# Kernel tuning notes

Measured on AMD Instinct MI355X. Metric: run time of the kernel, lower is better.

## Reference

```python
import jax, jax.numpy as jnp
import numpy as np

S, B, D, H = 2048, 2, 2048, 16
HD = D // H  # 128
EPS = 1e-5


def _layernorm(x, w, b):
    mu = jnp.mean(x, axis=-1, keepdims=True)
    var = jnp.mean((x - mu) ** 2, axis=-1, keepdims=True)
    return (x - mu) * jax.lax.rsqrt(var + EPS) * w + b


def _apply_rotary(x, freqs_cis):
    # x: [B, S, H, HD]; freqs_cis: [S, HD//2, 2]
    xr = x.astype(jnp.float32).reshape(x.shape[0], x.shape[1], x.shape[2], HD // 2, 2)
    f = freqs_cis.reshape(1, xr.shape[1], 1, xr.shape[3], 2)
    out = jnp.stack(
        [xr[..., 0] * f[..., 0] - xr[..., 1] * f[..., 1],
         xr[..., 1] * f[..., 0] + xr[..., 0] * f[..., 1]],
        axis=-1,
    )
    return out.reshape(x.shape).astype(x.dtype)


def setup_inputs() -> dict:
    key = jax.random.key(0)
    ks = jax.random.split(key, 6)
    scale = 0.02
    return {
        "x": jax.random.normal(ks[0], (S, B, D), dtype=jnp.float32),
        "freqs_cis": jax.random.normal(ks[1], (S, HD // 2, 2), dtype=jnp.float32),
        "wqkv_w": jax.random.normal(ks[2], (3 * D, D), dtype=jnp.float32) * scale,
        "wqkv_b": jnp.zeros((3 * D,), dtype=jnp.float32),
        "wo_w": jax.random.normal(ks[3], (D, D), dtype=jnp.float32) * scale,
        "wo_b": jnp.zeros((D,), dtype=jnp.float32),
        "qn_w": jnp.ones((HD,), dtype=jnp.float32),
        "qn_b": jnp.zeros((HD,), dtype=jnp.float32),
        "kn_w": jnp.ones((HD,), dtype=jnp.float32),
        "kn_b": jnp.zeros((HD,), dtype=jnp.float32),
    }


def reference(x, freqs_cis, wqkv_w, wqkv_b, wo_w, wo_b, qn_w, qn_b, kn_w, kn_b):
    # x: [S, B, D] -> [B, S, D]
    xb = jnp.transpose(x, (1, 0, 2))
    qkv = jnp.einsum("bsd,ed->bse", xb, wqkv_w) + wqkv_b  # [B, S, 3D]
    xq, xk, xv = jnp.split(qkv, 3, axis=-1)
    xq = xq.reshape(B, S, H, HD)
    xk = xk.reshape(B, S, H, HD)
    xv = xv.reshape(B, S, H, HD)
    # QK-norm over head_dim
    xq = _layernorm(xq, qn_w, qn_b)
    xk = _layernorm(xk, kn_w, kn_b)
    # RoPE
    xq = _apply_rotary(xq, freqs_cis)
    xk = _apply_rotary(xk, freqs_cis)
    # [B, H, S, HD]
    q = jnp.transpose(xq, (0, 2, 1, 3))
    k = jnp.transpose(xk, (0, 2, 1, 3))
    v = jnp.transpose(xv, (0, 2, 1, 3))
    scores = jnp.einsum("bhqd,bhkd->bhqk", q, k) / jnp.sqrt(jnp.float32(HD))
    causal = jnp.tril(jnp.ones((S, S), dtype=bool))
    scores = jnp.where(causal, scores, jnp.finfo(scores.dtype).min)
    attn = jax.nn.softmax(scores, axis=-1)
    out = jnp.einsum("bhqk,bhkd->bhqd", attn, v)  # [B, H, S, HD]
    out = jnp.transpose(out, (0, 2, 1, 3)).reshape(B, S, D)
    out = jnp.einsum("bsd,ed->bse", out, wo_w) + wo_b
    return jnp.transpose(out, (1, 0, 2))  # [S, B, D]
```

## Files before the change

kernel.cpp:

```cpp
#include <hip/hip_runtime.h>
#include <hip/hip_bf16.h>

#define S 2048
#define B 2
#define D 2048
#define H 16
#define HD 128
#define N3 6144
#define KD 2048

typedef __hip_bfloat16 bf16;
typedef float f32x4 __attribute__((ext_vector_type(4)));
typedef short short8 __attribute__((ext_vector_type(8)));
typedef short sv4 __attribute__((ext_vector_type(4)));

__device__ __forceinline__ void gload16(const void* g, void* l) {
    __builtin_amdgcn_global_load_lds((const __attribute__((address_space(1))) void*)g,
                                     (__attribute__((address_space(3))) void*)l, 16, 0, 0);
}
__device__ __forceinline__ void bar() {
    asm volatile("" ::: "memory");
    __builtin_amdgcn_s_barrier();
    asm volatile("" ::: "memory");
}

__global__ __launch_bounds__(256) void cvt_x_kernel(const float* __restrict__ x, bf16* __restrict__ xb) {
    int i = blockIdx.x * 256 + threadIdx.x;
    int d  = i & (D - 1);
    int sb = i >> 11;
    int b  = sb & (B - 1);
    int s  = sb >> 1;
    xb[((size_t)(b * S + s) << 11) + d] = __float2bfloat16(x[i]);
}

__global__ __launch_bounds__(256) void cvt_w_kernel(const float* __restrict__ in, bf16* __restrict__ o, int n) {
    for (int i = blockIdx.x * blockDim.x + threadIdx.x; i < n; i += gridDim.x * blockDim.x)
        o[i] = __float2bfloat16(in[i]);
}

template <int MODE>
__global__ __launch_bounds__(256, 2) void gemm128(
    const bf16* __restrict__ A, const bf16* __restrict__ W, const float* __restrict__ bias,
    bf16* __restrict__ oq, bf16* __restrict__ ok, bf16* __restrict__ ovT,
    float* __restrict__ oOut)
{
    constexpr int NT = KD / 64;

    __shared__ __align__(16) bf16 SA[2][128 * 64];
    __shared__ __align__(16) bf16 SB[2][128 * 64];

    const int tid = threadIdx.x;
    const int w = tid >> 6, l = tid & 63;
    const int wm = w >> 1, wn = w & 1;
    const int l15 = l & 15, l4 = l >> 4;

    const int nwg = gridDim.x * gridDim.y;
    const int id  = blockIdx.y * gridDim.x + blockIdx.x;
    const int nid = (id & 7) * (nwg >> 3) + (id >> 3);
    const int tileN = (nid % gridDim.x) * 128;
    const int tileM = (nid / gridDim.x) * 128;

    const int lrow8 = l >> 3;
    const int lsb   = ((l & 7) * 16) ^ (lrow8 << 4);
    const int rxor  = (l15 & 7) << 3;

    const char* AgT = (const char*)A + (size_t)tileM * (KD * 2);
    const char* WgT = (const char*)W + (size_t)tileN * (KD * 2);

    auto stage_tile = [&](int buf, int kt) {
#pragma unroll
        for (int j = 0; j < 4; ++j) {
            const int chunk = w * 4 + j;
            gload16(AgT + (size_t)(chunk * 8 + lrow8) * (KD * 2) + kt * 128 + lsb,
                    (char*)&SA[buf][0] + chunk * 1024);
        }
#pragma unroll
        for (int j = 0; j < 4; ++j) {
            const int chunk = w * 4 + j;
            gload16(WgT + (size_t)(chunk * 8 + lrow8) * (KD * 2) + kt * 128 + lsb,
                    (char*)&SB[buf][0] + chunk * 1024);
        }
    };

    f32x4 acc[4][4] = {};

#define TILE_BODY(BUF, KTN)                                                                \
    {                                                                                      \
        stage_tile(BUF ^ 1, KTN);                                                          \
        _Pragma("unroll") for (int kk = 0; kk < 2; ++kk) {                                 \
            short8 bfrag[4], afr[4];                                                       \
            _Pragma("unroll") for (int ni = 0; ni < 4; ++ni)                               \
                bfrag[ni] = *(const short8*)&SB[BUF][(wn * 64 + ni * 16 + l15) * 64 +      \
                                                     ((kk * 32 + l4 * 8) ^ rxor)];         \
            _Pragma("unroll") for (int q = 0; q < 4; ++q)                                  \
                afr[q] = *(const short8*)&SA[BUF][(wm * 64 + q * 16 + l15) * 64 +          \
                                                  ((kk * 32 + l4 * 8) ^ rxor)];            \
            __builtin_amdgcn_s_setprio(1);                                                 \
            _Pragma("unroll") for (int q = 0; q < 4; ++q)                                  \
                _Pragma("unroll") for (int ni = 0; ni < 4; ++ni)                           \
                    acc[q][ni] = __builtin_amdgcn_mfma_f32_16x16x32_bf16(                  \
                        afr[q], bfrag[ni], acc[q][ni], 0, 0, 0);                           \
            __builtin_amdgcn_s_setprio(0);                                                 \
        }                                                                                  \
        asm volatile("s_waitcnt vmcnt(0)" ::: "memory");                                   \
        bar();                                                                             \
    }

    stage_tile(0, 0);
    asm volatile("s_waitcnt vmcnt(0)" ::: "memory");
    bar();

#pragma unroll 1
    for (int t = 0; t < NT; t += 2) {
        const int tn1 = (t + 1 < NT) ? t + 1 : NT - 1;
        const int tn2 = (t + 2 < NT) ? t + 2 : NT - 1;
        TILE_BODY(0, tn1)
        TILE_BODY(1, tn2)
    }
#undef TILE_BODY

#pragma unroll
    for (int mi = 0; mi < 4; ++mi) {
#pragma unroll
        for (int ni = 0; ni < 4; ++ni) {
            const int ncol = tileN + wn * 64 + ni * 16 + l15;
            const float bv = bias[ncol];
            const int m0 = tileM + wm * 64 + mi * 16 + l4 * 4;
            if (MODE == 0) {
                const int b_ = m0 >> 11, s0 = m0 & (S - 1);
                const int which = ncol >> 11;
                const int hh = (ncol >> 7) & (H - 1);
                const int hd = ncol & (HD - 1);
                const int bh = b_ * H + hh;
                if (which == 2) {
                    sv4 pk;
#pragma unroll
                    for (int r = 0; r < 4; ++r) {
                        __hip_bfloat16 t = __float2bfloat16(acc[mi][ni][r] + bv);
                        pk[r] = reinterpret_cast<short&>(t);
                    }
                    *(sv4*)&ovT[((size_t)bh * HD + hd) * S + s0] = pk;
                } else {
                    bf16* dst = which ? ok : oq;
#pragma unroll
                    for (int r = 0; r < 4; ++r)
                        dst[((size_t)bh * S + s0 + r) * HD + hd] =
                            __float2bfloat16(acc[mi][ni][r] + bv);
                }
            } else {
#pragma unroll
                for (int r = 0; r < 4; ++r) {
                    const int m = m0 + r;
                    const int b_ = m >> 11, s_ = m & (S - 1);
                    oOut[((size_t)s_ * B + b_) * D + ncol] = acc[mi][ni][r] + bv;
                }
            }
        }
    }
}

__global__ __launch_bounds__(256) void ln_rope_kernel(
    bf16* __restrict__ q, bf16* __restrict__ k,
    const float* __restrict__ fc,
    const float* __restrict__ qw, const float* __restrict__ qb,
    const float* __restrict__ kw, const float* __restrict__ kb)
{
    const int tid = threadIdx.x;
    const int w = tid >> 6, l = tid & 63;
    const int row = blockIdx.x * 4 + w;
    const int s_ = row & (S - 1);
    const size_t base = (size_t)row * HD;
    const float f0 = fc[s_ * HD + 2 * l];
    const float f1 = fc[s_ * HD + 2 * l + 1];

#pragma unroll
    for (int which = 0; which < 2; ++which) {
        bf16* p = which == 0 ? q : k;
        const float* gw = which == 0 ? qw : kw;
        const float* gb = which == 0 ? qb : kb;
        const float osc = which == 0 ? 0.08838834764831845f : 1.0f;
        float x0 = __bfloat162float(p[base + 2 * l]);
        float x1 = __bfloat162float(p[base + 2 * l + 1]);
        float sm = x0 + x1;
#pragma unroll
        for (int msk = 1; msk < 64; msk <<= 1) sm += __shfl_xor(sm, msk);
        const float mu = sm * (1.0f / HD);
        const float d0 = x0 - mu, d1 = x1 - mu;
        float vs = d0 * d0 + d1 * d1;
#pragma unroll
        for (int msk = 1; msk < 64; msk <<= 1) vs += __shfl_xor(vs, msk);
        const float rstd = rsqrtf(vs * (1.0f / HD) + 1e-5f);
        const float n0 = d0 * rstd * gw[2 * l] + gb[2 * l];
        const float n1 = d1 * rstd * gw[2 * l + 1] + gb[2 * l + 1];
        p[base + 2 * l]     = __float2bfloat16((n0 * f0 - n1 * f1) * osc);
        p[base + 2 * l + 1] = __float2bfloat16((n1 * f0 + n0 * f1) * osc);
    }
}

__global__ __launch_bounds__(256, 2) void attn_kernel(
    const bf16* __restrict__ q, const bf16* __restrict__ k, const bf16* __restrict__ vT,
    bf16* __restrict__ out)
{
    __shared__ __align__(16) bf16 KT[2][64 * 128];
    __shared__ __align__(16) bf16 VS[2][128 * 64];
    __shared__ __align__(16) bf16 Pb[4][16 * 72];

    const int tid = threadIdx.x, w = tid >> 6, l = tid & 63;
    const int l15 = l & 15, l4 = l >> 4;

    const int id  = blockIdx.y * gridDim.x + blockIdx.x;
    const int nid = (id & 7) * 128 + (id >> 3);
    const int bh  = nid >> 5;
    const int qt  = 31 - (nid & 31);

    const int b_ = bh >> 4, hh = bh & (H - 1);
    const int qbase = qt * 64;
    const int qr0 = qbase + w * 16;
    const size_t hQ = (size_t)bh * S * HD;
    const size_t hV = (size_t)bh * HD * S;

    const char* kbase = (const char*)(k + hQ);
    const char* vbase = (const char*)(vT + hV);
    int ksrc[4], vsrc[4], kdst[4], vdst[4];
#pragma unroll
    for (int j = 0; j < 4; ++j) {
        const int ik = w * 4 + j;
        const int rt = ik * 4 + (l >> 4);
        ksrc[j] = rt * 256 + (((l & 15) * 16) ^ ((rt & 15) << 4));
        kdst[j] = ik * 1024;
        const int rd = ik * 8 + (l >> 3);
        vsrc[j] = rd * (S * 2) + (((l & 7) * 16) ^ ((rd & 7) << 4));
        vdst[j] = ik * 1024;
    }

    short8 aq[4];
#pragma unroll
    for (int c = 0; c < 4; ++c)
        aq[c] = *(const short8*)&q[hQ + (size_t)(qr0 + l15) * HD + c * 32 + l4 * 8];

    f32x4 o[8] = {};
    float psum[4] = {0.0f, 0.0f, 0.0f, 0.0f};

#pragma unroll
    for (int j = 0; j < 4; ++j)
        gload16(kbase + ksrc[j], (char*)KT[0] + kdst[j]);

    const int kx = l15 << 3;
    const int vx = (l15 & 7) << 3;
    const float LOG2E = 1.4426950408889634f;
    const float SHIFT = -23.083120654223414f;

    for (int kvt = 0; kvt <= qt; ++kvt) {
        const int kvb = kvt * 64;
        const int cur = kvt & 1;
#pragma unroll
        for (int j = 0; j < 4; ++j)
            gload16(vbase + (size_t)kvb * 2 + vsrc[j], (char*)VS[cur] + vdst[j]);
        if (kvt < qt) {
#pragma unroll
            for (int j = 0; j < 4; ++j)
                gload16(kbase + (size_t)(kvb + 64) * 256 + ksrc[j], (char*)KT[cur ^ 1] + kdst[j]);
        }
        if (kvt < qt) { asm volatile("s_waitcnt vmcnt(8)" ::: "memory"); }
        else          { asm volatile("s_waitcnt vmcnt(4)" ::: "memory"); }
        bar();

        f32x4 sacc[4] = {};
#pragma unroll
        for (int c = 0; c < 4; ++c) {
            const int cole = (c * 32 + l4 * 8) ^ kx;
#pragma unroll
            for (int n = 0; n < 4; ++n) {
                short8 bk = *(const short8*)&KT[cur][(n * 16 + l15) * 128 + cole];
                sacc[n] = __builtin_amdgcn_mfma_f32_16x16x32_bf16(aq[c], bk, sacc[n], 0, 0, 0);
            }
        }

        if (kvb == qbase) {
#pragma unroll
            for (int n = 0; n < 4; ++n)
#pragma unroll
                for (int r = 0; r < 4; ++r) {
                    float sv = (kvb + n * 16 + l15 > qr0 + l4 * 4 + r) ? -1e30f : sacc[n][r];
                    const float pv = __builtin_amdgcn_exp2f(__builtin_fmaf(sv, LOG2E, SHIFT));
                    sacc[n][r] = pv;
                    psum[r] += pv;
                }
        } else {
#pragma unroll
            for (int n = 0; n < 4; ++n)
#pragma unroll
                for (int r = 0; r < 4; ++r) {
                    const float pv = __builtin_amdgcn_exp2f(__builtin_fmaf(sacc[n][r], LOG2E, SHIFT));
                    sacc[n][r] = pv;
                    psum[r] += pv;
                }
        }

#pragma unroll
        for (int n = 0; n < 4; ++n)
#pragma unroll
            for (int r = 0; r < 4; ++r)
                Pb[w][(l4 * 4 + r) * 72 + n * 16 + l15] = __float2bfloat16(sacc[n][r]);
        short8 ap[2];
#pragma unroll
        for (int c = 0; c < 2; ++c)
            ap[c] = *(const short8*)&Pb[w][l15 * 72 + c * 32 + l4 * 8];

        if (kvt < qt) { asm volatile("s_waitcnt vmcnt(4)" ::: "memory"); }
        else          { asm volatile("s_waitcnt vmcnt(0)" ::: "memory"); }
        bar();

#pragma unroll
        for (int c = 0; c < 2; ++c) {
#pragma unroll
            for (int d = 0; d < 8; ++d) {
                const int rd = d * 16 + l15;
                short8 bv = *(const short8*)&VS[cur][rd * 64 + ((c * 32 + l4 * 8) ^ vx)];
                o[d] = __builtin_amdgcn_mfma_f32_16x16x32_bf16(ap[c], bv, o[d], 0, 0, 0);
            }
        }
    }

#pragma unroll
    for (int r = 0; r < 4; ++r) {
#pragma unroll
        for (int msk = 1; msk < 16; msk <<= 1) psum[r] += __shfl_xor(psum[r], msk);
        const float inv = 1.0f / psum[r];
        const int s_ = qr0 + l4 * 4 + r;
        const size_t obase = ((size_t)b_ * S + s_) * D + hh * HD;
#pragma unroll
        for (int d = 0; d < 8; ++d)
            out[obase + d * 16 + l15] = __float2bfloat16(o[d][r] * inv);
    }
}

extern "C" void kernel_launch(void* const* d_in, const int* in_sizes, int n_in,
                              void* d_out, int out_size, void* d_ws, size_t ws_size,
                              hipStream_t stream) {
    const float* x      = (const float*)d_in[0];
    const float* fc     = (const float*)d_in[1];
    const float* wqkv_w = (const float*)d_in[2];
    const float* wqkv_b = (const float*)d_in[3];
    const float* wo_w   = (const float*)d_in[4];
    const float* wo_b   = (const float*)d_in[5];
    const float* qn_w   = (const float*)d_in[6];
    const float* qn_b   = (const float*)d_in[7];
    const float* kn_w   = (const float*)d_in[8];
    const float* kn_b   = (const float*)d_in[9];
    float* out = (float*)d_out;
    char* ws = (char*)d_ws;

    bf16* xb = (bf16*)(ws);
    bf16* w1 = (bf16*)(ws + 16777216);
    bf16* wo = (bf16*)(ws + 41943040);
    bf16* qb = (bf16*)(ws + 50331648);
    bf16* kb = (bf16*)(ws + 67108864);
    bf16* vT = (bf16*)(ws + 83886080);
    bf16* ao = (bf16*)(ws + 100663296);

    cvt_x_kernel<<<(S * B * D) / 256, 256, 0, stream>>>(x, xb);
    cvt_w_kernel<<<4096, 256, 0, stream>>>(wqkv_w, w1, N3 * D);
    cvt_w_kernel<<<2048, 256, 0, stream>>>(wo_w, wo, D * D);

    gemm128<0><<<dim3(N3 / 128, (B * S) / 128), 256, 0, stream>>>(
        xb, w1, wqkv_b, qb, kb, vT, nullptr);

    ln_rope_kernel<<<(B * H * S) / 4, 256, 0, stream>>>(qb, kb, fc, qn_w, qn_b, kn_w, kn_b);

    attn_kernel<<<dim3(S / 64, B * H), 256, 0, stream>>>(qb, kb, vT, ao);

    gemm128<1><<<dim3(D / 128, (B * S) / 128), 256, 0, stream>>>(
        ao, wo, wo_b, nullptr, nullptr, nullptr, out);
}
```

Baseline: 286.0 us.

## Pair causal query tiles per block to balance work and share K/V loads

```diff
diff --git a/kernel.cpp b/kernel.cpp
--- a/kernel.cpp
+++ b/kernel.cpp
@@ -209,13 +209,15 @@
     const int l15 = l & 15, l4 = l >> 4;
 
     const int id  = blockIdx.y * gridDim.x + blockIdx.x;
-    const int nid = (id & 7) * 128 + (id >> 3);
-    const int bh  = nid >> 5;
-    const int qt  = 31 - (nid & 31);
+    const int nid = (id & 7) * 64 + (id >> 3);
+    const int bh  = nid >> 4;
+    const int pr  = nid & 15;
+    const int qtA = 31 - pr;
+    const int qtB = pr;
 
     const int b_ = bh >> 4, hh = bh & (H - 1);
-    const int qbase = qt * 64;
-    const int qr0 = qbase + w * 16;
+    const int qrA = qtA * 64 + w * 16;
+    const int qrB = qtB * 64 + w * 16;
     const size_t hQ = (size_t)bh * S * HD;
     const size_t hV = (size_t)bh * HD * S;
 
@@ -233,13 +235,15 @@
         vdst[j] = ik * 1024;
     }
 
-    short8 aq[4];
-#pragma unroll
-    for (int c = 0; c < 4; ++c)
-        aq[c] = *(const short8*)&q[hQ + (size_t)(qr0 + l15) * HD + c * 32 + l4 * 8];
-
-    f32x4 o[8] = {};
-    float psum[4] = {0.0f, 0.0f, 0.0f, 0.0f};
+    short8 aqA[4], aqB[4];
+#pragma unroll
+    for (int c = 0; c < 4; ++c) {
+        aqA[c] = *(const short8*)&q[hQ + (size_t)(qrA + l15) * HD + c * 32 + l4 * 8];
+        aqB[c] = *(const short8*)&q[hQ + (size_t)(qrB + l15) * HD + c * 32 + l4 * 8];
+    }
+
+    f32x4 oA[8] = {}, oB[8] = {};
+    float psA[4] = {0.f, 0.f, 0.f, 0.f}, psB[4] = {0.f, 0.f, 0.f, 0.f};
 
 #pragma unroll
     for (int j = 0; j < 4; ++j)
@@ -250,65 +254,102 @@
     const float LOG2E = 1.4426950408889634f;
     const float SHIFT = -23.083120654223414f;
 
-    for (int kvt = 0; kvt <= qt; ++kvt) {
+    for (int kvt = 0; kvt <= qtA; ++kvt) {
         const int kvb = kvt * 64;
         const int cur = kvt & 1;
+        const bool doB = (kvt <= qtB);
 #pragma unroll
         for (int j = 0; j < 4; ++j)
             gload16(vbase + (size_t)kvb * 2 + vsrc[j], (char*)VS[cur] + vdst[j]);
-        if (kvt < qt) {
+        if (kvt < qtA) {
 #pragma unroll
             for (int j = 0; j < 4; ++j)
                 gload16(kbase + (size_t)(kvb + 64) * 256 + ksrc[j], (char*)KT[cur ^ 1] + kdst[j]);
         }
-        if (kvt < qt) { asm volatile("s_waitcnt vmcnt(8)" ::: "memory"); }
-        else          { asm volatile("s_waitcnt vmcnt(4)" ::: "memory"); }
+        if (kvt < qtA) { asm volatile("s_waitcnt vmcnt(8)" ::: "memory"); }
+        else           { asm volatile("s_waitcnt vmcnt(4)" ::: "memory"); }
         bar();
 
-        f32x4 sacc[4] = {};
-#pragma unroll
-        for (int c = 0; c < 4; ++c) {
-            const int cole = (c * 32 + l4 * 8) ^ kx;
-#pragma unroll
-            for (int n = 0; n < 4; ++n) {
-                short8 bk = *(const short8*)&KT[cur][(n * 16 + l15) * 128 + cole];
-                sacc[n] = __builtin_amdgcn_mfma_f32_16x16x32_bf16(aq[c], bk, sacc[n], 0, 0, 0);
-            }
-        }
-
-        if (kvb == qbase) {
+        short8 apA[2], apB[2];
+        {
+            f32x4 sacc[4] = {};
+#pragma unroll
+            for (int c = 0; c < 4; ++c) {
+                const int cole = (c * 32 + l4 * 8) ^ kx;
+#pragma unroll
+                for (int n = 0; n < 4; ++n) {
+                    short8 bk = *(const short8*)&KT[cur][(n * 16 + l15) * 128 + cole];
+                    sacc[n] = __builtin_amdgcn_mfma_f32_16x16x32_bf16(aqA[c], bk, sacc[n], 0, 0, 0);
+                }
+            }
+            if (kvt == qtA) {
+#pragma unroll
+                for (int n = 0; n < 4; ++n)
+#pragma unroll
+                    for (int r = 0; r < 4; ++r) {
+                        float sv = (kvb + n * 16 + l15 > qrA + l4 * 4 + r) ? -1e30f : sacc[n][r];
+                        const float pv = __builtin_amdgcn_exp2f(__builtin_fmaf(sv, LOG2E, SHIFT));
+                        sacc[n][r] = pv; psA[r] += pv;
+                    }
+            } else {
+#pragma unroll
+                for (int n = 0; n < 4; ++n)
+#pragma unroll
+                    for (int r = 0; r < 4; ++r) {
+                        const float pv = __builtin_amdgcn_exp2f(__builtin_fmaf(sacc[n][r], LOG2E, SHIFT));
+                        sacc[n][r] = pv; psA[r] += pv;
+                    }
+            }
 #pragma unroll
             for (int n = 0; n < 4; ++n)
 #pragma unroll
-                for (int r = 0; r < 4; ++r) {
-                    float sv = (kvb + n * 16 + l15 > qr0 + l4 * 4 + r) ? -1e30f : sacc[n][r];
-                    const float pv = __builtin_amdgcn_exp2f(__builtin_fmaf(sv, LOG2E, SHIFT));
-                    sacc[n][r] = pv;
-                    psum[r] += pv;
+                for (int r = 0; r < 4; ++r)
+                    Pb[w][(l4 * 4 + r) * 72 + n * 16 + l15] = __float2bfloat16(sacc[n][r]);
+#pragma unroll
+            for (int c = 0; c < 2; ++c)
+                apA[c] = *(const short8*)&Pb[w][l15 * 72 + c * 32 + l4 * 8];
+        }
+        if (doB) {
+            f32x4 sacc[4] = {};
+#pragma unroll
+            for (int c = 0; c < 4; ++c) {
+                const int cole = (c * 32 + l4 * 8) ^ kx;
+#pragma unroll
+                for (int n = 0; n < 4; ++n) {
+                    short8 bk = *(const short8*)&KT[cur][(n * 16 + l15) * 128 + cole];
+                    sacc[n] = __builtin_amdgcn_mfma_f32_16x16x32_bf16(aqB[c], bk, sacc[n], 0, 0, 0);
                 }
-        } else {
+            }
+            if (kvt == qtB) {
+#pragma unroll
+                for (int n = 0; n < 4; ++n)
+#pragma unroll
+                    for (int r = 0; r < 4; ++r) {
+                        float sv = (kvb + n * 16 + l15 > qrB + l4 * 4 + r) ? -1e30f : sacc[n][r];
+                        const float pv = __builtin_amdgcn_exp2f(__builtin_fmaf(sv, LOG2E, SHIFT));
+                        sacc[n][r] = pv; psB[r] += pv;
+                    }
+            } else {
+#pragma unroll
+                for (int n = 0; n < 4; ++n)
+#pragma unroll
+                    for (int r = 0; r < 4; ++r) {
+                        const float pv = __builtin_amdgcn_exp2f(__builtin_fmaf(sacc[n][r], LOG2E, SHIFT));
+                        sacc[n][r] = pv; psB[r] += pv;
+                    }
+            }
 #pragma unroll
             for (int n = 0; n < 4; ++n)
 #pragma unroll
-                for (int r = 0; r < 4; ++r) {
-                    const float pv = __builtin_amdgcn_exp2f(__builtin_fmaf(sacc[n][r], LOG2E, SHIFT));
-                    sacc[n][r] = pv;
-                    psum[r] += pv;
-                }
-        }
-
-#pragma unroll
-        for (int n = 0; n < 4; ++n)
-#pragma unroll
-            for (int r = 0; r < 4; ++r)
-                Pb[w][(l4 * 4 + r) * 72 + n * 16 + l15] = __float2bfloat16(sacc[n][r]);
-        short8 ap[2];
-#pragma unroll
-        for (int c = 0; c < 2; ++c)
-            ap[c] = *(const short8*)&Pb[w][l15 * 72 + c * 32 + l4 * 8];
-
-        if (kvt < qt) { asm volatile("s_waitcnt vmcnt(4)" ::: "memory"); }
-        else          { asm volatile("s_waitcnt vmcnt(0)" ::: "memory"); }
+                for (int r = 0; r < 4; ++r)
+                    Pb[w][(l4 * 4 + r) * 72 + n * 16 + l15] = __float2bfloat16(sacc[n][r]);
+#pragma unroll
+            for (int c = 0; c < 2; ++c)
+                apB[c] = *(const short8*)&Pb[w][l15 * 72 + c * 32 + l4 * 8];
+        }
+
+        if (kvt < qtA) { asm volatile("s_waitcnt vmcnt(4)" ::: "memory"); }
+        else           { asm volatile("s_waitcnt vmcnt(0)" ::: "memory"); }
         bar();
 
 #pragma unroll
@@ -317,7 +358,18 @@
             for (int d = 0; d < 8; ++d) {
                 const int rd = d * 16 + l15;
                 short8 bv = *(const short8*)&VS[cur][rd * 64 + ((c * 32 + l4 * 8) ^ vx)];
-                o[d] = __builtin_amdgcn_mfma_f32_16x16x32_bf16(ap[c], bv, o[d], 0, 0, 0);
+                oA[d] = __builtin_amdgcn_mfma_f32_16x16x32_bf16(apA[c], bv, oA[d], 0, 0, 0);
+            }
+        }
+        if (doB) {
+#pragma unroll
+            for (int c = 0; c < 2; ++c) {
+#pragma unroll
+                for (int d = 0; d < 8; ++d) {
+                    const int rd = d * 16 + l15;
+                    short8 bv = *(const short8*)&VS[cur][rd * 64 + ((c * 32 + l4 * 8) ^ vx)];
+                    oB[d] = __builtin_amdgcn_mfma_f32_16x16x32_bf16(apB[c], bv, oB[d], 0, 0, 0);
+                }
             }
         }
     }
@@ -325,13 +377,24 @@
 #pragma unroll
     for (int r = 0; r < 4; ++r) {
 #pragma unroll
-        for (int msk = 1; msk < 16; msk <<= 1) psum[r] += __shfl_xor(psum[r], msk);
-        const float inv = 1.0f / psum[r];
-        const int s_ = qr0 + l4 * 4 + r;
+        for (int msk = 1; msk < 16; msk <<= 1) psA[r] += __shfl_xor(psA[r], msk);
+        const float inv = 1.0f / psA[r];
+        const int s_ = qrA + l4 * 4 + r;
         const size_t obase = ((size_t)b_ * S + s_) * D + hh * HD;
 #pragma unroll
         for (int d = 0; d < 8; ++d)
-            out[obase + d * 16 + l15] = __float2bfloat16(o[d][r] * inv);
+            out[obase + d * 16 + l15] = __float2bfloat16(oA[d][r] * inv);
+    }
+#pragma unroll
+    for (int r = 0; r < 4; ++r) {
+#pragma unroll
+        for (int msk = 1; msk < 16; msk <<= 1) psB[r] += __shfl_xor(psB[r], msk);
+        const float inv = 1.0f / psB[r];
+        const int s_ = qrB + l4 * 4 + r;
+        const size_t obase = ((size_t)b_ * S + s_) * D + hh * HD;
+#pragma unroll
+        for (int d = 0; d < 8; ++d)
+            out[obase + d * 16 + l15] = __float2bfloat16(oB[d][r] * inv);
     }
 }
 
@@ -368,7 +431,7 @@
 
     ln_rope_kernel<<<(B * H * S) / 4, 256, 0, stream>>>(qb, kb, fc, qn_w, qn_b, kn_w, kn_b);
 
-    attn_kernel<<<dim3(S / 64, B * H), 256, 0, stream>>>(qb, kb, vT, ao);
+    attn_kernel<<<dim3(16, B * H), 256, 0, stream>>>(qb, kb, vT, ao);
 
     gemm128<1><<<dim3(D / 128, (B * S) / 128), 256, 0, stream>>>(
         ao, wo, wo_b, nullptr, nullptr, nullptr, out);
```

After: 262.0 us. -8.4%, faster.
